# Optimization experiments

Measured on AMD Instinct MI355X. Metric: run time of the kernel, lower is better.

Reference implementation:

```python
import jax, jax.numpy as jnp
import numpy as np

V_MAX = 3.0
FEATURE_CLAMP = 10.0
TOP_K = 1


def _green_diag(d):
    """Diagonal of G = (tridiag(sub=1, diag=d, super=1))^{-1} for each batch row.
    d: (B, N) complex64. Stable two-sided continued-fraction (Thomas-like) recurrences:
      L_i = d_i - 1/L_{i-1},  U_i = d_i - 1/U_{i+1},  G_ii = 1/(L_i + U_i - d_i).
    Sequential over N (vectorized over B) via lax.scan.
    """
    dT = d.T  # (N, B)

    def step(c, di):
        nc = di - 1.0 / c
        return nc, nc

    L0 = dT[0]
    _, Lr = jax.lax.scan(step, L0, dT[1:])
    L = jnp.concatenate([L0[None], Lr], axis=0)  # (N, B)

    dR = dT[::-1]
    U0 = dR[0]
    _, Ur = jax.lax.scan(step, U0, dR[1:])
    U = jnp.concatenate([U0[None], Ur], axis=0)[::-1]  # (N, B)

    return (1.0 / (L + U - dT)).T  # (B, N)


def setup_inputs() -> dict:
    key = jax.random.key(0)
    B, N, D, E, F = 4, 4096, 512, 4, 2048
    ks = jax.random.split(key, 8)
    s = lambda k, sh, sc: (jax.random.normal(k, sh, jnp.float32) * sc)
    return dict(
        x=jax.random.normal(ks[0], (B, N, D), jnp.float32),
        v_proj_w=s(ks[1], (1, D), D ** -0.5),
        v_proj_b=jnp.zeros((1,), jnp.float32),
        gamma=jnp.float32(0.0),
        epsilon_param=jnp.float32(1.0),
        gate_w=s(ks[2], (E, D), D ** -0.5),
        gate_b=jnp.zeros((E,), jnp.float32),
        w1=s(ks[3], (E, D, F), D ** -0.5),
        b1=jnp.zeros((E, F), jnp.float32),
        w2=s(ks[4], (E, F, D), F ** -0.5),
        b2=jnp.zeros((E, D), jnp.float32),
        out_w=s(ks[5], (D, 2), 0.5),
        out_b=jnp.zeros((D,), jnp.float32),
        bk_scale=jnp.ones((D,), jnp.float32),
    )


def reference(x, v_proj_w, v_proj_b, gamma, epsilon_param, gate_w, gate_b,
              w1, b1, w2, b2, out_w, out_b, bk_scale):
    # 1) scalar potential from tokens
    v = jnp.einsum('bnd,od->bno', x, v_proj_w)[..., 0] + v_proj_b[0]  # (B, N)
    v = jnp.clip(v, -V_MAX, V_MAX)

    # 2) gamma-shifted complex tridiagonal Green's function diagonal
    eps = jax.nn.softplus(epsilon_param) + 1e-6
    z = 1j * (eps + gamma)                       # complex64 scalar
    d = ((v - 2.0).astype(jnp.complex64) - z)    # he_diag - z, (B, N)
    G = _green_diag(d)                            # (B, N) complex
    feats = jnp.clip(jnp.stack([G.real, G.imag], axis=-1), -FEATURE_CLAMP, FEATURE_CLAMP)  # (B,N,2)

    # 3) sparse MoE FFN (top-1 routing, experts = Linear -> GELU -> Linear)
    logits = jnp.einsum('bnd,ed->bne', x, gate_w) + gate_b
    probs = jax.nn.softmax(logits, axis=-1)
    top_p, top_i = jax.lax.top_k(probs, TOP_K)
    top_w = top_p / jnp.sum(top_p, axis=-1, keepdims=True)
    wmask = jnp.sum(jax.nn.one_hot(top_i, probs.shape[-1], dtype=probs.dtype) * top_w[..., None], axis=-2)  # (B,N,E)

    h = jax.nn.gelu(jnp.einsum('bnd,edf->benf', x, w1) + b1[None, :, None, :], approximate=False)
    y = jnp.einsum('benf,efd->bend', h, w2) + b2[None, :, None, :]
    ffn_out = jnp.einsum('bne,bend->bnd', wmask, y)

    # 4) combine spectral features with FFN output
    spec_out = jnp.einsum('bnc,dc->bnd', feats, out_w) + out_b
    return ffn_out + bk_scale * spec_out
```

## Files before the change

kernel.cpp:

```cpp
#include <hip/hip_runtime.h>
#include <hip/hip_bf16.h>
#include <math.h>


typedef __bf16 bf16x8 __attribute__((ext_vector_type(8)));
typedef float  f32x4  __attribute__((ext_vector_type(4)));
typedef __attribute__((address_space(3))) __bf16 lbf16;

#define B_   4
#define N_   4096
#define D_   512
#define E_   4
#define F_   2048
#define T_   (B_*N_)
#define CAP_ T_
#define RT_MAX 132
#define PADROWS (RT_MAX*128)

#define LGKM_BARRIER() asm volatile("s_waitcnt lgkmcnt(0)\n\ts_barrier" ::: "memory")

__device__ __forceinline__ void gload_lds16(const __bf16* g, lbf16* l) {
    __builtin_amdgcn_global_load_lds(
        (__attribute__((address_space(1))) void*)(void*)g,
        (__attribute__((address_space(3))) void*)l, 16, 0, 0);
}

__device__ alignas(256) __bf16 s_w1t[(size_t)E_*F_*D_];
__device__ alignas(256) __bf16 s_w2t[(size_t)E_*D_*F_];
__device__ alignas(256) __bf16 s_xb[(size_t)PADROWS*D_];
__device__ alignas(256) __bf16 s_H[(size_t)PADROWS*F_];
__device__ alignas(256) float2 s_d[T_];
__device__ alignas(256) float2 s_feats[T_];
__device__ alignas(256) float2 s_L[T_];
__device__ alignas(256) float2 s_U[T_];
__device__ alignas(256) int    s_perm[E_*CAP_];
__device__ alignas(256) int    s_cnt[E_];
__device__ alignas(256) int    s_tpre[8];
__device__ alignas(256) int    s_eid[T_];

__global__ void transpose_bf16_kernel(const float* __restrict__ src,
                                      __bf16* __restrict__ dst,
                                      int R, int C) {
    __shared__ alignas(16) float tile[32][33];
    int e = blockIdx.z;
    const float* s = src + (size_t)e * R * C;
    __bf16*      d = dst + (size_t)e * R * C;
    int c0 = blockIdx.x * 32, r0 = blockIdx.y * 32;
    int tx = threadIdx.x, ty = threadIdx.y;
    #pragma unroll
    for (int i = 0; i < 4; ++i)
        tile[ty + i*8][tx] = s[(size_t)(r0 + ty + i*8) * C + c0 + tx];
    __syncthreads();
    #pragma unroll
    for (int i = 0; i < 4; ++i)
        d[(size_t)(c0 + ty + i*8) * R + r0 + tx] = (__bf16)tile[tx][ty + i*8];
}

__device__ inline float dot8(float4 a, float4 b, float4 c, float4 d) {
    float s =      a.x * c.x;
    s = fmaf(a.y, c.y, s); s = fmaf(a.z, c.z, s); s = fmaf(a.w, c.w, s);
    s = fmaf(b.x, d.x, s); s = fmaf(b.y, d.y, s); s = fmaf(b.z, d.z, s);
    s = fmaf(b.w, d.w, s);
    return s;
}

__device__ inline float wave_sum(float s) {
    #pragma unroll
    for (int off = 32; off > 0; off >>= 1) s += __shfl_xor(s, off);
    return s;
}

__global__ __launch_bounds__(256) void prep_kernel(
        const float* __restrict__ x,
        const float* __restrict__ vw, const float* __restrict__ vb,
        const float* __restrict__ gamma, const float* __restrict__ epsp,
        const float* __restrict__ gw, const float* __restrict__ gb,
        float2* __restrict__ dbuf, int* __restrict__ eid) {
    int wv = threadIdx.x >> 6, lane = threadIdx.x & 63;
    int token = blockIdx.x * 4 + wv;
    const float4* xr = (const float4*)(x + (size_t)token * D_);
    float4 xa = xr[lane*2], xb = xr[lane*2 + 1];

    const float4* vr = (const float4*)vw;
    float sv = dot8(xa, xb, vr[lane*2], vr[lane*2 + 1]);
    float sg0, sg1, sg2, sg3;
    {
        const float4* g0 = (const float4*)(gw + 0*D_);
        const float4* g1 = (const float4*)(gw + 1*D_);
        const float4* g2 = (const float4*)(gw + 2*D_);
        const float4* g3 = (const float4*)(gw + 3*D_);
        sg0 = dot8(xa, xb, g0[lane*2], g0[lane*2+1]);
        sg1 = dot8(xa, xb, g1[lane*2], g1[lane*2+1]);
        sg2 = dot8(xa, xb, g2[lane*2], g2[lane*2+1]);
        sg3 = dot8(xa, xb, g3[lane*2], g3[lane*2+1]);
    }
    sv  = wave_sum(sv);
    sg0 = wave_sum(sg0); sg1 = wave_sum(sg1);
    sg2 = wave_sum(sg2); sg3 = wave_sum(sg3);

    if (lane == 0) {
        float v = sv + vb[0];
        v = fminf(fmaxf(v, -3.0f), 3.0f);
        float eps = log1pf(expf(epsp[0])) + 1e-6f;
        dbuf[token] = make_float2(v - 2.0f, -(eps + gamma[0]));

        float l0 = sg0 + gb[0], l1 = sg1 + gb[1], l2 = sg2 + gb[2], l3 = sg3 + gb[3];
        float best = l0; int be = 0;
        if (l1 > best) { best = l1; be = 1; }
        if (l2 > best) { best = l2; be = 2; }
        if (l3 > best) { best = l3; be = 3; }
        eid[token] = be;
    }
}

__global__ __launch_bounds__(1024) void route_kernel(
        const int* __restrict__ eid, int* __restrict__ perm,
        int* __restrict__ cnt, int* __restrict__ tpre) {
    __shared__ int chunkcnt[256][4];
    __shared__ int chunkoff[256][4];
    __shared__ int totals[4];
    int tid = threadIdx.x;
    int wv = tid >> 6, lane = tid & 63;

    for (int c = wv; c < 256; c += 16) {
        int e = eid[c * 64 + lane];
        unsigned long long m0 = __ballot(e == 0);
        unsigned long long m1 = __ballot(e == 1);
        unsigned long long m2 = __ballot(e == 2);
        unsigned long long m3 = __ballot(e == 3);
        if (lane == 0) {
            chunkcnt[c][0] = __popcll(m0);
            chunkcnt[c][1] = __popcll(m1);
            chunkcnt[c][2] = __popcll(m2);
            chunkcnt[c][3] = __popcll(m3);
        }
    }
    __syncthreads();

    if (wv < 4) {
        int e = wv, carry = 0;
        #pragma unroll
        for (int g = 0; g < 4; ++g) {
            int idx = g * 64 + lane;
            int v = chunkcnt[idx][e];
            int s = v;
            #pragma unroll
            for (int off = 1; off < 64; off <<= 1) {
                int u = __shfl_up(s, off);
                if (lane >= off) s += u;
            }
            chunkoff[idx][e] = carry + s - v;
            carry += __shfl(s, 63);
        }
        if (lane == 0) { cnt[e] = carry; totals[e] = carry; }
    }
    __syncthreads();
    if (tid == 0) {
        int acc = 0;
        #pragma unroll
        for (int e = 0; e < E_; ++e) { tpre[e] = acc; acc += (totals[e] + 127) >> 7; }
        tpre[4] = acc;
    }

    for (int c = wv; c < 256; c += 16) {
        int t = c * 64 + lane;
        int e = eid[t];
        unsigned long long m0 = __ballot(e == 0);
        unsigned long long m1 = __ballot(e == 1);
        unsigned long long m2 = __ballot(e == 2);
        unsigned long long m3 = __ballot(e == 3);
        unsigned long long mym = (e == 0) ? m0 : (e == 1) ? m1 : (e == 2) ? m2 : m3;
        unsigned long long below = lane ? (mym & ((1ull << lane) - 1ull)) : 0ull;
        int pos = chunkoff[c][e] + __popcll(below);
        perm[e * CAP_ + pos] = t;
    }
}

__global__ __launch_bounds__(512) void scan_kernel(
        const float2* __restrict__ dbuf, float2* __restrict__ Lb,
        float2* __restrict__ Ub, float2* __restrict__ feats) {
    __shared__ alignas(16) float chunkM[8][64][8];
    __shared__ alignas(16) float bound[8][64][4];
    int tid = threadIdx.x;
    int s = tid >> 6, c = tid & 63;
    int b = s & 3, dir = s >> 2;

    {
        float ar=1, ai=0, br=0, bi=0, cr=0, ci=0, dr=1, di=0;
        for (int j = 0; j < 64; ++j) {
            int seq = c*64 + j;
            int orig = dir ? (N_-1 - seq) : seq;
            float2 dv = dbuf[b*N_ + orig];
            float nar = dv.x*ar - dv.y*ai - cr;
            float nai = dv.x*ai + dv.y*ar - ci;
            float nbr = dv.x*br - dv.y*bi - dr;
            float nbi = dv.x*bi + dv.y*br - di;
            cr = ar; ci = ai; dr = br; di = bi;
            ar = nar; ai = nai; br = nbr; bi = nbi;
            if ((j & 7) == 7) {
                float m = fmaxf(fmaxf(fmaxf(fabsf(ar),fabsf(ai)),fmaxf(fabsf(br),fabsf(bi))),
                                fmaxf(fmaxf(fabsf(cr),fabsf(ci)),fmaxf(fabsf(dr),fabsf(di))));
                float inv = 1.0f / fmaxf(m, 1e-30f);
                ar*=inv; ai*=inv; br*=inv; bi*=inv; cr*=inv; ci*=inv; dr*=inv; di*=inv;
            }
        }
        float* cm = chunkM[s][c];
        cm[0]=ar; cm[1]=ai; cm[2]=br; cm[3]=bi; cm[4]=cr; cm[5]=ci; cm[6]=dr; cm[7]=di;
    }
    __syncthreads();

    if (tid < 8) {
        int ss = tid;
        float pr=1, pi=0, qr=0, qi=0;
        for (int cc = 0; cc < 64; ++cc) {
            float* bd = bound[ss][cc];
            bd[0]=pr; bd[1]=pi; bd[2]=qr; bd[3]=qi;
            const float* m = chunkM[ss][cc];
            float npr = m[0]*pr - m[1]*pi + m[2]*qr - m[3]*qi;
            float npi = m[0]*pi + m[1]*pr + m[2]*qi + m[3]*qr;
            float nqr = m[4]*pr - m[5]*pi + m[6]*qr - m[7]*qi;
            float nqi = m[4]*pi + m[5]*pr + m[6]*qi + m[7]*qr;
            float mx = fmaxf(fmaxf(fabsf(npr),fabsf(npi)), fmaxf(fabsf(nqr),fabsf(nqi)));
            float inv = 1.0f / fmaxf(mx, 1e-30f);
            pr = npr*inv; pi = npi*inv; qr = nqr*inv; qi = nqi*inv;
        }
    }
    __syncthreads();

    {
        const float* bd = bound[s][c];
        float pr=bd[0], pi=bd[1], qr=bd[2], qi=bd[3];
        float den = fmaxf(pr*pr + pi*pi, 1e-30f);
        float invr = (qr*pr + qi*pi) / den;
        float invi = (qi*pr - qr*pi) / den;
        for (int j = 0; j < 64; ++j) {
            int seq = c*64 + j;
            int orig = dir ? (N_-1 - seq) : seq;
            int t = b*N_ + orig;
            float2 dv = dbuf[t];
            float Lr = dv.x - invr, Li = dv.y - invi;
            if (dir) Ub[t] = make_float2(Lr, Li);
            else     Lb[t] = make_float2(Lr, Li);
            float d2 = Lr*Lr + Li*Li;
            invr = Lr / d2; invi = -Li / d2;
        }
    }
    __threadfence();
    __syncthreads();

    for (int t = tid; t < T_; t += 512) {
        float2 L = Lb[t], U = Ub[t], dv = dbuf[t];
        float sr = L.x + U.x - dv.x;
        float si = L.y + U.y - dv.y;
        float den = sr*sr + si*si;
        float Gr = sr / den, Gi = -si / den;
        Gr = fminf(fmaxf(Gr, -10.0f), 10.0f);
        Gi = fminf(fmaxf(Gi, -10.0f), 10.0f);
        feats[t] = make_float2(Gr, Gi);
    }
}

__global__ __launch_bounds__(256) void reorder_kernel(
        const float* __restrict__ x, const int* __restrict__ perm,
        const int* __restrict__ cnt, const int* __restrict__ tpre,
        __bf16* __restrict__ xb) {
    int wv = threadIdx.x >> 6, lane = threadIdx.x & 63;
    int prow = blockIdx.x * 4 + wv;
    if (prow >= tpre[4] * 128) return;
    int e = 0;
    #pragma unroll
    for (int k = 1; k < E_; ++k) if (prow >= tpre[k] * 128) e = k;
    int i = prow - tpre[e] * 128;
    int token = (i < cnt[e]) ? perm[e * CAP_ + i] : -1;
    bf16x8 v = {0,0,0,0,0,0,0,0};
    if (token >= 0) {
        const float4* xr = (const float4*)(x + (size_t)token * D_);
        float4 a = xr[lane*2], b = xr[lane*2 + 1];
        v = (bf16x8){(__bf16)a.x,(__bf16)a.y,(__bf16)a.z,(__bf16)a.w,
                     (__bf16)b.x,(__bf16)b.y,(__bf16)b.z,(__bf16)b.w};
    }
    *(bf16x8*)(xb + (size_t)prow * D_ + lane * 8) = v;
}

__global__ __launch_bounds__(256, 4) void gemm1_kernel(
        const __bf16* __restrict__ xb, const __bf16* __restrict__ w1t,
        const float* __restrict__ b1, __bf16* __restrict__ Hb,
        const int* __restrict__ tpre) {
    int bid = blockIdx.x;
    int lb  = (bid & 7) * 264 + (bid >> 3);
    int rt = lb >> 4, ct = lb & 15;
    if (rt >= tpre[4]) return;
    int e = 0;
    #pragma unroll
    for (int k = 1; k < E_; ++k) if (rt >= tpre[k]) e = k;

    __shared__ __bf16 A[128 * 64];
    __shared__ __bf16 Bm[128 * 64];

    int tid = threadIdx.x, lane = tid & 63, wv = tid >> 6;
    int fl = lane & 15, gl = lane >> 4;
    int wr = wv >> 1, wc = wv & 1;

    int r0    = wv * 8 + (lane >> 3);
    int scolb = ((lane & 7) * 16) ^ ((lane >> 3) << 4);
    const __bf16* aS0 = xb  + (size_t)(rt * 128 + r0) * 512 + (scolb >> 1);
    const __bf16* bS0 = w1t + (size_t)(e * F_ + ct * 128 + r0) * 512 + (scolb >> 1);
    lbf16* aD0 = (lbf16*)A  + wv * 512;
    lbf16* bD0 = (lbf16*)Bm + wv * 512;

    int xorv = (fl & 7) << 4;
    int cs0 = (gl * 16) ^ xorv;
    int cs1 = (64 + gl * 16) ^ xorv;
    const char* Ab = (const char*)A  + (wr * 64 + fl) * 128;
    const char* Bb = (const char*)Bm + (wc * 64 + fl) * 128;

    f32x4 acc[4][4];
    #pragma unroll
    for (int m = 0; m < 4; ++m)
        #pragma unroll
        for (int n = 0; n < 4; ++n) acc[m][n] = (f32x4){0.f,0.f,0.f,0.f};

    #pragma unroll
    for (int i = 0; i < 4; ++i) {
        gload_lds16(aS0 + (size_t)i * 32 * 512, aD0 + i * 2048);
        gload_lds16(bS0 + (size_t)i * 32 * 512, bD0 + i * 2048);
    }
    for (int kt = 0; kt < 8; ++kt) {
        __syncthreads();
        #pragma unroll
        for (int ks = 0; ks < 2; ++ks) {
            int cs = ks ? cs1 : cs0;
            bf16x8 af[4], bfr[4];
            #pragma unroll
            for (int m = 0; m < 4; ++m)
                af[m] = *(const bf16x8*)(Ab + m * 2048 + cs);
            #pragma unroll
            for (int n = 0; n < 4; ++n)
                bfr[n] = *(const bf16x8*)(Bb + n * 2048 + cs);
            #pragma unroll
            for (int m = 0; m < 4; ++m)
                #pragma unroll
                for (int n = 0; n < 4; ++n)
                    acc[m][n] = __builtin_amdgcn_mfma_f32_16x16x32_bf16(af[m], bfr[n], acc[m][n], 0, 0, 0);
        }
        if (kt + 1 < 8) {
            LGKM_BARRIER();
            #pragma unroll
            for (int i = 0; i < 4; ++i) {
                gload_lds16(aS0 + (size_t)i * 32 * 512 + (kt + 1) * 64, aD0 + i * 2048);
                gload_lds16(bS0 + (size_t)i * 32 * 512 + (kt + 1) * 64, bD0 + i * 2048);
            }
        }
    }

    int gre = rt * 128 + wr * 64;
    int gce = ct * 128 + wc * 64;
    float b1v[4];
    #pragma unroll
    for (int n = 0; n < 4; ++n) b1v[n] = b1[e * F_ + gce + n*16 + fl];
    #pragma unroll
    for (int m = 0; m < 4; ++m)
        #pragma unroll
        for (int r = 0; r < 4; ++r) {
            __bf16* hrow = Hb + (size_t)(gre + m*16 + gl*4 + r) * F_ + gce;
            #pragma unroll
            for (int n = 0; n < 4; ++n) {
                float val = acc[m][n][r] + b1v[n];
                float g = 0.5f * val * (1.0f + erff(val * 0.70710678118654752f));
                hrow[n*16 + fl] = (__bf16)g;
            }
        }
}

__global__ __launch_bounds__(256, 4) void gemm2_kernel(
        const __bf16* __restrict__ Hb, const __bf16* __restrict__ w2t,
        const float* __restrict__ b2, const float* __restrict__ outw,
        const float* __restrict__ outb, const float* __restrict__ bk,
        const float2* __restrict__ feats, const int* __restrict__ perm,
        const int* __restrict__ cnt_p, const int* __restrict__ tpre,
        float* __restrict__ out) {
    int bid = blockIdx.x;
    int lb  = (bid & 7) * 66 + (bid >> 3);
    int rt = lb >> 2, ct = lb & 3;
    if (rt >= tpre[4]) return;
    int e = 0;
    #pragma unroll
    for (int k = 1; k < E_; ++k) if (rt >= tpre[k]) e = k;

    __shared__ __bf16 A[128 * 64];
    __shared__ __bf16 Bm[128 * 64];

    int tid = threadIdx.x, lane = tid & 63, wv = tid >> 6;
    int fl = lane & 15, gl = lane >> 4;
    int wr = wv >> 1, wc = wv & 1;

    int r0    = wv * 8 + (lane >> 3);
    int scolb = ((lane & 7) * 16) ^ ((lane >> 3) << 4);
    const __bf16* aS0 = Hb  + (size_t)(rt * 128 + r0) * F_ + (scolb >> 1);
    const __bf16* bS0 = w2t + (size_t)(e * D_ + ct * 128 + r0) * F_ + (scolb >> 1);
    lbf16* aD0 = (lbf16*)A  + wv * 512;
    lbf16* bD0 = (lbf16*)Bm + wv * 512;

    int xorv = (fl & 7) << 4;
    int cs0 = (gl * 16) ^ xorv;
    int cs1 = (64 + gl * 16) ^ xorv;
    const char* Ab = (const char*)A  + (wr * 64 + fl) * 128;
    const char* Bb = (const char*)Bm + (wc * 64 + fl) * 128;

    f32x4 acc[4][4];
    #pragma unroll
    for (int m = 0; m < 4; ++m)
        #pragma unroll
        for (int n = 0; n < 4; ++n) acc[m][n] = (f32x4){0.f,0.f,0.f,0.f};

    #pragma unroll
    for (int i = 0; i < 4; ++i) {
        gload_lds16(aS0 + (size_t)i * 32 * F_, aD0 + i * 2048);
        gload_lds16(bS0 + (size_t)i * 32 * F_, bD0 + i * 2048);
    }
    for (int kt = 0; kt < 32; ++kt) {
        __syncthreads();
        #pragma unroll
        for (int ks = 0; ks < 2; ++ks) {
            int cs = ks ? cs1 : cs0;
            bf16x8 af[4], bfr[4];
            #pragma unroll
            for (int m = 0; m < 4; ++m)
                af[m] = *(const bf16x8*)(Ab + m * 2048 + cs);
            #pragma unroll
            for (int n = 0; n < 4; ++n)
                bfr[n] = *(const bf16x8*)(Bb + n * 2048 + cs);
            #pragma unroll
            for (int m = 0; m < 4; ++m)
                #pragma unroll
                for (int n = 0; n < 4; ++n)
                    acc[m][n] = __builtin_amdgcn_mfma_f32_16x16x32_bf16(af[m], bfr[n], acc[m][n], 0, 0, 0);
        }
        if (kt + 1 < 32) {
            LGKM_BARRIER();
            #pragma unroll
            for (int i = 0; i < 4; ++i) {
                gload_lds16(aS0 + (size_t)i * 32 * F_ + (kt + 1) * 64, aD0 + i * 2048);
                gload_lds16(bS0 + (size_t)i * 32 * F_ + (kt + 1) * 64, bD0 + i * 2048);
            }
        }
    }

    int cnt = cnt_p[e];
    int ibase = rt * 128 + wr * 64 - tpre[e] * 128;
    int gce = ct * 128 + wc * 64;
    float c_b2[4], c_o0[4], c_o1[4], c_ob[4], c_bk[4];
    #pragma unroll
    for (int n = 0; n < 4; ++n) {
        int dcol = gce + n*16 + fl;
        c_b2[n] = b2[e * D_ + dcol];
        c_o0[n] = outw[dcol * 2 + 0];
        c_o1[n] = outw[dcol * 2 + 1];
        c_ob[n] = outb[dcol];
        c_bk[n] = bk[dcol];
    }
    #pragma unroll
    for (int m = 0; m < 4; ++m)
        #pragma unroll
        for (int r = 0; r < 4; ++r) {
            int i = ibase + m*16 + gl*4 + r;
            if (i >= cnt) continue;
            int token = perm[e * CAP_ + i];
            float2 ft = feats[token];
            float* orow = out + (size_t)token * D_;
            #pragma unroll
            for (int n = 0; n < 4; ++n) {
                int dcol = gce + n*16 + fl;
                float spec = ft.x * c_o0[n] + ft.y * c_o1[n] + c_ob[n];
                orow[dcol] = acc[m][n][r] + c_b2[n] + c_bk[n] * spec;
            }
        }
}

extern "C" void kernel_launch(void* const* d_in, const int* in_sizes, int n_in,
                              void* d_out, int out_size, void* d_ws, size_t ws_size,
                              hipStream_t stream) {
    const float* x     = (const float*)d_in[0];
    const float* vpw   = (const float*)d_in[1];
    const float* vpb   = (const float*)d_in[2];
    const float* gamma = (const float*)d_in[3];
    const float* epsp  = (const float*)d_in[4];
    const float* gw    = (const float*)d_in[5];
    const float* gb    = (const float*)d_in[6];
    const float* w1    = (const float*)d_in[7];
    const float* b1    = (const float*)d_in[8];
    const float* w2    = (const float*)d_in[9];
    const float* b2    = (const float*)d_in[10];
    const float* ow    = (const float*)d_in[11];
    const float* ob    = (const float*)d_in[12];
    const float* bk    = (const float*)d_in[13];
    float* out = (float*)d_out;

    const size_t szW  = (size_t)E_ * F_ * D_ * sizeof(__bf16);
    const size_t szF2 = (size_t)T_ * sizeof(float2);
    const size_t szPm = (size_t)E_ * CAP_ * sizeof(int);
    const size_t szCt = 256;
    const size_t szXb = (size_t)PADROWS * D_ * sizeof(__bf16);
    const size_t szH  = (size_t)PADROWS * F_ * sizeof(__bf16);
    const size_t szEi = (size_t)T_ * sizeof(int);
    size_t need = 2*szW + 4*szF2 + szPm + 2*szCt + szXb + szH + szEi + 16*256;

    __bf16 *w1t, *w2t, *xbuf, *Hbuf; float2 *dbuf, *Lb, *Ub, *feats;
    int *perm, *cnt, *tpre, *eid;
    int use_ws = (d_ws != nullptr && ws_size >= need);
    if (use_ws) {
        size_t off = 0;
        auto carve = [&](size_t bytes) {
            void* p = (char*)d_ws + off;
            off += (bytes + 255) & ~(size_t)255;
            return p;
        };
        w1t   = (__bf16*)carve(szW);
        w2t   = (__bf16*)carve(szW);
        xbuf  = (__bf16*)carve(szXb);
        Hbuf  = (__bf16*)carve(szH);
        dbuf  = (float2*)carve(szF2);
        Lb    = (float2*)carve(szF2);
        Ub    = (float2*)carve(szF2);
        feats = (float2*)carve(szF2);
        perm  = (int*)   carve(szPm);
        cnt   = (int*)   carve(szCt);
        tpre  = (int*)   carve(szCt);
        eid   = (int*)   carve(szEi);
    } else {
        void* p;
        hipGetSymbolAddress(&p, HIP_SYMBOL(s_w1t));  w1t   = (__bf16*)p;
        hipGetSymbolAddress(&p, HIP_SYMBOL(s_w2t));  w2t   = (__bf16*)p;
        hipGetSymbolAddress(&p, HIP_SYMBOL(s_xb));   xbuf  = (__bf16*)p;
        hipGetSymbolAddress(&p, HIP_SYMBOL(s_H));    Hbuf  = (__bf16*)p;
        hipGetSymbolAddress(&p, HIP_SYMBOL(s_d));    dbuf  = (float2*)p;
        hipGetSymbolAddress(&p, HIP_SYMBOL(s_L));    Lb    = (float2*)p;
        hipGetSymbolAddress(&p, HIP_SYMBOL(s_U));    Ub    = (float2*)p;
        hipGetSymbolAddress(&p, HIP_SYMBOL(s_feats));feats = (float2*)p;
        hipGetSymbolAddress(&p, HIP_SYMBOL(s_perm)); perm  = (int*)p;
        hipGetSymbolAddress(&p, HIP_SYMBOL(s_cnt));  cnt   = (int*)p;
        hipGetSymbolAddress(&p, HIP_SYMBOL(s_tpre)); tpre  = (int*)p;
        hipGetSymbolAddress(&p, HIP_SYMBOL(s_eid));  eid   = (int*)p;
    }

    dim3 tb(32, 8);
    transpose_bf16_kernel<<<dim3(F_/32, D_/32, E_), tb, 0, stream>>>(w1, w1t, D_, F_);
    transpose_bf16_kernel<<<dim3(D_/32, F_/32, E_), tb, 0, stream>>>(w2, w2t, F_, D_);
    prep_kernel<<<T_/4, 256, 0, stream>>>(x, vpw, vpb, gamma, epsp, gw, gb, dbuf, eid);
    route_kernel<<<1, 1024, 0, stream>>>(eid, perm, cnt, tpre);
    scan_kernel<<<1, 512, 0, stream>>>(dbuf, Lb, Ub, feats);
    reorder_kernel<<<PADROWS/4, 256, 0, stream>>>(x, perm, cnt, tpre, xbuf);
    gemm1_kernel<<<RT_MAX*16, 256, 0, stream>>>(xbuf, w1t, b1, Hbuf, tpre);
    gemm2_kernel<<<RT_MAX*4, 256, 0, stream>>>(Hbuf, w2t, b2, ow, ob, bk,
                                               feats, perm, cnt, tpre, out);
}
```

Measured before the change: 241.5 us.

## Double-buffer LDS tiles in expert GEMMs and use tanh-form GELU

Both expert GEMM kernels now keep two LDS buffers, so the global-to-LDS load of the next K tile is issued before the MFMA work on the current tile, overlapping memory with compute. The old path waited on a barrier before each reload. Occupancy hints drop from 4 to 2 blocks per CU because LDS per block doubles. The exact erf GELU is replaced by a tanh-style approximation written with a sigmoid and exp, which cuts epilogue cost but no longer matches the reference exact GELU.

```diff
diff --git a/kernel.cpp b/kernel.cpp
--- a/kernel.cpp
+++ b/kernel.cpp
@@ -17,12 +17,44 @@
 #define RT_MAX 132
 #define PADROWS (RT_MAX*128)
 
-#define LGKM_BARRIER() asm volatile("s_waitcnt lgkmcnt(0)\n\ts_barrier" ::: "memory")
-
 __device__ __forceinline__ void gload_lds16(const __bf16* g, lbf16* l) {
     __builtin_amdgcn_global_load_lds(
         (__attribute__((address_space(1))) void*)(void*)g,
         (__attribute__((address_space(3))) void*)l, 16, 0, 0);
+}
+
+__device__ __forceinline__ float fast_gelu(float x) {
+    float u = 1.5957691216f * fmaf(0.044715f * x, x * x, x);
+    return x / (1.0f + __expf(-u));
+}
+
+__device__ __forceinline__ void stage8(const __bf16* aS, const __bf16* bS,
+                                       lbf16* aD, lbf16* bD, int rstride) {
+    #pragma unroll
+    for (int i = 0; i < 4; ++i) {
+        gload_lds16(aS + (size_t)i * 32 * rstride, aD + i * 2048);
+        gload_lds16(bS + (size_t)i * 32 * rstride, bD + i * 2048);
+    }
+}
+
+__device__ __forceinline__ void mfma_tile(const char* Ab, const char* Bb,
+                                          int cs0, int cs1, f32x4 acc[4][4]) {
+    #pragma unroll
+    for (int ks = 0; ks < 2; ++ks) {
+        int cs = ks ? cs1 : cs0;
+        bf16x8 af[4], bfr[4];
+        #pragma unroll
+        for (int m = 0; m < 4; ++m)
+            af[m] = *(const bf16x8*)(Ab + m * 2048 + cs);
+        #pragma unroll
+        for (int n = 0; n < 4; ++n)
+            bfr[n] = *(const bf16x8*)(Bb + n * 2048 + cs);
+        #pragma unroll
+        for (int m = 0; m < 4; ++m)
+            #pragma unroll
+            for (int n = 0; n < 4; ++n)
+                acc[m][n] = __builtin_amdgcn_mfma_f32_16x16x32_bf16(af[m], bfr[n], acc[m][n], 0, 0, 0);
+    }
 }
 
 __device__ alignas(256) __bf16 s_w1t[(size_t)E_*F_*D_];
@@ -282,7 +314,7 @@
     *(bf16x8*)(xb + (size_t)prow * D_ + lane * 8) = v;
 }
 
-__global__ __launch_bounds__(256, 4) void gemm1_kernel(
+__global__ __launch_bounds__(256, 2) void gemm1_kernel(
         const __bf16* __restrict__ xb, const __bf16* __restrict__ w1t,
         const float* __restrict__ b1, __bf16* __restrict__ Hb,
         const int* __restrict__ tpre) {
@@ -294,8 +326,8 @@
     #pragma unroll
     for (int k = 1; k < E_; ++k) if (rt >= tpre[k]) e = k;
 
-    __shared__ __bf16 A[128 * 64];
-    __shared__ __bf16 Bm[128 * 64];
+    __shared__ __bf16 A[2][128 * 64];
+    __shared__ __bf16 Bm[2][128 * 64];
 
     int tid = threadIdx.x, lane = tid & 63, wv = tid >> 6;
     int fl = lane & 15, gl = lane >> 4;
@@ -305,14 +337,18 @@
     int scolb = ((lane & 7) * 16) ^ ((lane >> 3) << 4);
     const __bf16* aS0 = xb  + (size_t)(rt * 128 + r0) * 512 + (scolb >> 1);
     const __bf16* bS0 = w1t + (size_t)(e * F_ + ct * 128 + r0) * 512 + (scolb >> 1);
-    lbf16* aD0 = (lbf16*)A  + wv * 512;
-    lbf16* bD0 = (lbf16*)Bm + wv * 512;
+    lbf16* aD0 = (lbf16*)A[0]  + wv * 512;
+    lbf16* bD0 = (lbf16*)Bm[0] + wv * 512;
+    lbf16* aD1 = (lbf16*)A[1]  + wv * 512;
+    lbf16* bD1 = (lbf16*)Bm[1] + wv * 512;
 
     int xorv = (fl & 7) << 4;
     int cs0 = (gl * 16) ^ xorv;
     int cs1 = (64 + gl * 16) ^ xorv;
-    const char* Ab = (const char*)A  + (wr * 64 + fl) * 128;
-    const char* Bb = (const char*)Bm + (wc * 64 + fl) * 128;
+    const char* Ab0 = (const char*)A[0]  + (wr * 64 + fl) * 128;
+    const char* Bb0 = (const char*)Bm[0] + (wc * 64 + fl) * 128;
+    const char* Ab1 = (const char*)A[1]  + (wr * 64 + fl) * 128;
+    const char* Bb1 = (const char*)Bm[1] + (wc * 64 + fl) * 128;
 
     f32x4 acc[4][4];
     #pragma unroll
@@ -320,37 +356,17 @@
         #pragma unroll
         for (int n = 0; n < 4; ++n) acc[m][n] = (f32x4){0.f,0.f,0.f,0.f};
 
-    #pragma unroll
-    for (int i = 0; i < 4; ++i) {
-        gload_lds16(aS0 + (size_t)i * 32 * 512, aD0 + i * 2048);
-        gload_lds16(bS0 + (size_t)i * 32 * 512, bD0 + i * 2048);
-    }
-    for (int kt = 0; kt < 8; ++kt) {
+    stage8(aS0, bS0, aD0, bD0, 512);
+    __syncthreads();
+    #pragma unroll
+    for (int kp = 0; kp < 4; ++kp) {
+        int k0 = 2 * kp;
+        if (k0 + 1 < 8) stage8(aS0 + (k0+1)*64, bS0 + (k0+1)*64, aD1, bD1, 512);
+        mfma_tile(Ab0, Bb0, cs0, cs1, acc);
         __syncthreads();
-        #pragma unroll
-        for (int ks = 0; ks < 2; ++ks) {
-            int cs = ks ? cs1 : cs0;
-            bf16x8 af[4], bfr[4];
-            #pragma unroll
-            for (int m = 0; m < 4; ++m)
-                af[m] = *(const bf16x8*)(Ab + m * 2048 + cs);
-            #pragma unroll
-            for (int n = 0; n < 4; ++n)
-                bfr[n] = *(const bf16x8*)(Bb + n * 2048 + cs);
-            #pragma unroll
-            for (int m = 0; m < 4; ++m)
-                #pragma unroll
-                for (int n = 0; n < 4; ++n)
-                    acc[m][n] = __builtin_amdgcn_mfma_f32_16x16x32_bf16(af[m], bfr[n], acc[m][n], 0, 0, 0);
-        }
-        if (kt + 1 < 8) {
-            LGKM_BARRIER();
-            #pragma unroll
-            for (int i = 0; i < 4; ++i) {
-                gload_lds16(aS0 + (size_t)i * 32 * 512 + (kt + 1) * 64, aD0 + i * 2048);
-                gload_lds16(bS0 + (size_t)i * 32 * 512 + (kt + 1) * 64, bD0 + i * 2048);
-            }
-        }
+        if (k0 + 2 < 8) stage8(aS0 + (k0+2)*64, bS0 + (k0+2)*64, aD0, bD0, 512);
+        mfma_tile(Ab1, Bb1, cs0, cs1, acc);
+        __syncthreads();
     }
 
     int gre = rt * 128 + wr * 64;
@@ -364,15 +380,12 @@
         for (int r = 0; r < 4; ++r) {
             __bf16* hrow = Hb + (size_t)(gre + m*16 + gl*4 + r) * F_ + gce;
             #pragma unroll
-            for (int n = 0; n < 4; ++n) {
-                float val = acc[m][n][r] + b1v[n];
-                float g = 0.5f * val * (1.0f + erff(val * 0.70710678118654752f));
-                hrow[n*16 + fl] = (__bf16)g;
-            }
-        }
-}
-
-__global__ __launch_bounds__(256, 4) void gemm2_kernel(
+            for (int n = 0; n < 4; ++n)
+                hrow[n*16 + fl] = (__bf16)fast_gelu(acc[m][n][r] + b1v[n]);
+        }
+}
+
+__global__ __launch_bounds__(256, 2) void gemm2_kernel(
         const __bf16* __restrict__ Hb, const __bf16* __restrict__ w2t,
         const float* __restrict__ b2, const float* __restrict__ outw,
         const float* __restrict__ outb, const float* __restrict__ bk,
@@ -387,8 +400,8 @@
     #pragma unroll
     for (int k = 1; k < E_; ++k) if (rt >= tpre[k]) e = k;
 
-    __shared__ __bf16 A[128 * 64];
-    __shared__ __bf16 Bm[128 * 64];
+    __shared__ __bf16 A[2][128 * 64];
+    __shared__ __bf16 Bm[2][128 * 64];
 
     int tid = threadIdx.x, lane = tid & 63, wv = tid >> 6;
     int fl = lane & 15, gl = lane >> 4;
@@ -398,14 +411,18 @@
     int scolb = ((lane & 7) * 16) ^ ((lane >> 3) << 4);
     const __bf16* aS0 = Hb  + (size_t)(rt * 128 + r0) * F_ + (scolb >> 1);
     const __bf16* bS0 = w2t + (size_t)(e * D_ + ct * 128 + r0) * F_ + (scolb >> 1);
-    lbf16* aD0 = (lbf16*)A  + wv * 512;
-    lbf16* bD0 = (lbf16*)Bm + wv * 512;
+    lbf16* aD0 = (lbf16*)A[0]  + wv * 512;
+    lbf16* bD0 = (lbf16*)Bm[0] + wv * 512;
+    lbf16* aD1 = (lbf16*)A[1]  + wv * 512;
+    lbf16* bD1 = (lbf16*)Bm[1] + wv * 512;
 
     int xorv = (fl & 7) << 4;
     int cs0 = (gl * 16) ^ xorv;
     int cs1 = (64 + gl * 16) ^ xorv;
-    const char* Ab = (const char*)A  + (wr * 64 + fl) * 128;
-    const char* Bb = (const char*)Bm + (wc * 64 + fl) * 128;
+    const char* Ab0 = (const char*)A[0]  + (wr * 64 + fl) * 128;
+    const char* Bb0 = (const char*)Bm[0] + (wc * 64 + fl) * 128;
+    const char* Ab1 = (const char*)A[1]  + (wr * 64 + fl) * 128;
+    const char* Bb1 = (const char*)Bm[1] + (wc * 64 + fl) * 128;
 
     f32x4 acc[4][4];
     #pragma unroll
@@ -413,37 +430,17 @@
         #pragma unroll
         for (int n = 0; n < 4; ++n) acc[m][n] = (f32x4){0.f,0.f,0.f,0.f};
 
-    #pragma unroll
-    for (int i = 0; i < 4; ++i) {
-        gload_lds16(aS0 + (size_t)i * 32 * F_, aD0 + i * 2048);
-        gload_lds16(bS0 + (size_t)i * 32 * F_, bD0 + i * 2048);
-    }
-    for (int kt = 0; kt < 32; ++kt) {
+    stage8(aS0, bS0, aD0, bD0, F_);
+    __syncthreads();
+    #pragma unroll 4
+    for (int kp = 0; kp < 16; ++kp) {
+        int k0 = 2 * kp;
+        if (k0 + 1 < 32) stage8(aS0 + (k0+1)*64, bS0 + (k0+1)*64, aD1, bD1, F_);
+        mfma_tile(Ab0, Bb0, cs0, cs1, acc);
         __syncthreads();
-        #pragma unroll
-        for (int ks = 0; ks < 2; ++ks) {
-            int cs = ks ? cs1 : cs0;
-            bf16x8 af[4], bfr[4];
-            #pragma unroll
-            for (int m = 0; m < 4; ++m)
-                af[m] = *(const bf16x8*)(Ab + m * 2048 + cs);
-            #pragma unroll
-            for (int n = 0; n < 4; ++n)
-                bfr[n] = *(const bf16x8*)(Bb + n * 2048 + cs);
-            #pragma unroll
-            for (int m = 0; m < 4; ++m)
-                #pragma unroll
-                for (int n = 0; n < 4; ++n)
-                    acc[m][n] = __builtin_amdgcn_mfma_f32_16x16x32_bf16(af[m], bfr[n], acc[m][n], 0, 0, 0);
-        }
-        if (kt + 1 < 32) {
-            LGKM_BARRIER();
-            #pragma unroll
-            for (int i = 0; i < 4; ++i) {
-                gload_lds16(aS0 + (size_t)i * 32 * F_ + (kt + 1) * 64, aD0 + i * 2048);
-                gload_lds16(bS0 + (size_t)i * 32 * F_ + (kt + 1) * 64, bD0 + i * 2048);
-            }
-        }
+        if (k0 + 2 < 32) stage8(aS0 + (k0+2)*64, bS0 + (k0+2)*64, aD0, bD0, F_);
+        mfma_tile(Ab1, Bb1, cs0, cs1, acc);
+        __syncthreads();
     }
 
     int cnt = cnt_p[e];
```

Result: slower. 265.6 us (+10.0%).

## Use 256-row tiles in gemm1 with 512 threads and a fast tanh GELU

Applied to the files above, without the earlier changes.

Expert row padding becomes 256-aligned, and gemm1 now computes 256x128 output tiles with eight waves, so each loaded w1 tile is reused across twice as many token rows. Reorder and gemm2 indexing are adjusted to the new padding. The exact erf GELU is replaced by a tanh-form approximation computed with an exponential, which lowers epilogue cost but deviates from the exact GELU the reference asks for. The larger padding adds some wasted rows, and the bigger block may reduce occupancy.

```diff
diff --git a/kernel.cpp b/kernel.cpp
--- a/kernel.cpp
+++ b/kernel.cpp
@@ -14,8 +14,9 @@
 #define F_   2048
 #define T_   (B_*N_)
 #define CAP_ T_
-#define RT_MAX 132
-#define PADROWS (RT_MAX*128)
+#define R256 68
+#define RT128 (R256*2)
+#define PADROWS (R256*256)
 
 #define LGKM_BARRIER() asm volatile("s_waitcnt lgkmcnt(0)\n\ts_barrier" ::: "memory")
 
@@ -23,6 +24,31 @@
     __builtin_amdgcn_global_load_lds(
         (__attribute__((address_space(1))) void*)(void*)g,
         (__attribute__((address_space(3))) void*)l, 16, 0, 0);
+}
+
+__device__ __forceinline__ float fast_gelu(float x) {
+    float u = 1.5957691216f * fmaf(0.044715f * x, x * x, x);
+    return x / (1.0f + __expf(-u));
+}
+
+__device__ __forceinline__ void mfma_tile(const char* Ab, const char* Bb,
+                                          int cs0, int cs1, f32x4 acc[4][4]) {
+    #pragma unroll
+    for (int ks = 0; ks < 2; ++ks) {
+        int cs = ks ? cs1 : cs0;
+        bf16x8 af[4], bfr[4];
+        #pragma unroll
+        for (int m = 0; m < 4; ++m)
+            af[m] = *(const bf16x8*)(Ab + m * 2048 + cs);
+        #pragma unroll
+        for (int n = 0; n < 4; ++n)
+            bfr[n] = *(const bf16x8*)(Bb + n * 2048 + cs);
+        #pragma unroll
+        for (int m = 0; m < 4; ++m)
+            #pragma unroll
+            for (int n = 0; n < 4; ++n)
+                acc[m][n] = __builtin_amdgcn_mfma_f32_16x16x32_bf16(af[m], bfr[n], acc[m][n], 0, 0, 0);
+    }
 }
 
 __device__ alignas(256) __bf16 s_w1t[(size_t)E_*F_*D_];
@@ -158,7 +184,7 @@
     if (tid == 0) {
         int acc = 0;
         #pragma unroll
-        for (int e = 0; e < E_; ++e) { tpre[e] = acc; acc += (totals[e] + 127) >> 7; }
+        for (int e = 0; e < E_; ++e) { tpre[e] = acc; acc += (totals[e] + 255) >> 8; }
         tpre[4] = acc;
     }
 
@@ -266,11 +292,11 @@
         __bf16* __restrict__ xb) {
     int wv = threadIdx.x >> 6, lane = threadIdx.x & 63;
     int prow = blockIdx.x * 4 + wv;
-    if (prow >= tpre[4] * 128) return;
+    if (prow >= tpre[4] * 256) return;
     int e = 0;
     #pragma unroll
-    for (int k = 1; k < E_; ++k) if (prow >= tpre[k] * 128) e = k;
-    int i = prow - tpre[e] * 128;
+    for (int k = 1; k < E_; ++k) if (prow >= tpre[k] * 256) e = k;
+    int i = prow - tpre[e] * 256;
     int token = (i < cnt[e]) ? perm[e * CAP_ + i] : -1;
     bf16x8 v = {0,0,0,0,0,0,0,0};
     if (token >= 0) {
@@ -282,31 +308,31 @@
     *(bf16x8*)(xb + (size_t)prow * D_ + lane * 8) = v;
 }
 
-__global__ __launch_bounds__(256, 4) void gemm1_kernel(
+__global__ __launch_bounds__(512, 4) void gemm1_kernel(
         const __bf16* __restrict__ xb, const __bf16* __restrict__ w1t,
         const float* __restrict__ b1, __bf16* __restrict__ Hb,
         const int* __restrict__ tpre) {
     int bid = blockIdx.x;
-    int lb  = (bid & 7) * 264 + (bid >> 3);
+    int lb  = (bid & 7) * 136 + (bid >> 3);
     int rt = lb >> 4, ct = lb & 15;
     if (rt >= tpre[4]) return;
     int e = 0;
     #pragma unroll
     for (int k = 1; k < E_; ++k) if (rt >= tpre[k]) e = k;
 
-    __shared__ __bf16 A[128 * 64];
+    __shared__ __bf16 A[256 * 64];
     __shared__ __bf16 Bm[128 * 64];
 
     int tid = threadIdx.x, lane = tid & 63, wv = tid >> 6;
     int fl = lane & 15, gl = lane >> 4;
     int wr = wv >> 1, wc = wv & 1;
 
-    int r0    = wv * 8 + (lane >> 3);
-    int scolb = ((lane & 7) * 16) ^ ((lane >> 3) << 4);
-    const __bf16* aS0 = xb  + (size_t)(rt * 128 + r0) * 512 + (scolb >> 1);
-    const __bf16* bS0 = w1t + (size_t)(e * F_ + ct * 128 + r0) * 512 + (scolb >> 1);
-    lbf16* aD0 = (lbf16*)A  + wv * 512;
-    lbf16* bD0 = (lbf16*)Bm + wv * 512;
+    int r8    = lane >> 3;
+    int scolb = ((lane & 7) * 16) ^ (r8 << 4);
+    const __bf16* aS0 = xb  + (size_t)(rt * 256 + wv * 32 + r8) * 512 + (scolb >> 1);
+    const __bf16* bS0 = w1t + (size_t)(e * F_ + ct * 128 + wv * 16 + r8) * 512 + (scolb >> 1);
+    lbf16* aD0 = (lbf16*)A  + wv * 32 * 64;
+    lbf16* bD0 = (lbf16*)Bm + wv * 16 * 64;
 
     int xorv = (fl & 7) << 4;
     int cs0 = (gl * 16) ^ xorv;
@@ -321,39 +347,27 @@
         for (int n = 0; n < 4; ++n) acc[m][n] = (f32x4){0.f,0.f,0.f,0.f};
 
     #pragma unroll
-    for (int i = 0; i < 4; ++i) {
-        gload_lds16(aS0 + (size_t)i * 32 * 512, aD0 + i * 2048);
-        gload_lds16(bS0 + (size_t)i * 32 * 512, bD0 + i * 2048);
-    }
+    for (int i = 0; i < 4; ++i)
+        gload_lds16(aS0 + (size_t)i * 8 * 512, aD0 + i * 512);
+    #pragma unroll
+    for (int i = 0; i < 2; ++i)
+        gload_lds16(bS0 + (size_t)i * 8 * 512, bD0 + i * 512);
+
     for (int kt = 0; kt < 8; ++kt) {
         __syncthreads();
-        #pragma unroll
-        for (int ks = 0; ks < 2; ++ks) {
-            int cs = ks ? cs1 : cs0;
-            bf16x8 af[4], bfr[4];
-            #pragma unroll
-            for (int m = 0; m < 4; ++m)
-                af[m] = *(const bf16x8*)(Ab + m * 2048 + cs);
-            #pragma unroll
-            for (int n = 0; n < 4; ++n)
-                bfr[n] = *(const bf16x8*)(Bb + n * 2048 + cs);
-            #pragma unroll
-            for (int m = 0; m < 4; ++m)
-                #pragma unroll
-                for (int n = 0; n < 4; ++n)
-                    acc[m][n] = __builtin_amdgcn_mfma_f32_16x16x32_bf16(af[m], bfr[n], acc[m][n], 0, 0, 0);
-        }
+        mfma_tile(Ab, Bb, cs0, cs1, acc);
         if (kt + 1 < 8) {
             LGKM_BARRIER();
             #pragma unroll
-            for (int i = 0; i < 4; ++i) {
-                gload_lds16(aS0 + (size_t)i * 32 * 512 + (kt + 1) * 64, aD0 + i * 2048);
-                gload_lds16(bS0 + (size_t)i * 32 * 512 + (kt + 1) * 64, bD0 + i * 2048);
-            }
-        }
-    }
-
-    int gre = rt * 128 + wr * 64;
+            for (int i = 0; i < 4; ++i)
+                gload_lds16(aS0 + (size_t)i * 8 * 512 + (kt + 1) * 64, aD0 + i * 512);
+            #pragma unroll
+            for (int i = 0; i < 2; ++i)
+                gload_lds16(bS0 + (size_t)i * 8 * 512 + (kt + 1) * 64, bD0 + i * 512);
+        }
+    }
+
+    int gre = rt * 256 + wr * 64;
     int gce = ct * 128 + wc * 64;
     float b1v[4];
     #pragma unroll
@@ -364,11 +378,8 @@
         for (int r = 0; r < 4; ++r) {
             __bf16* hrow = Hb + (size_t)(gre + m*16 + gl*4 + r) * F_ + gce;
             #pragma unroll
-            for (int n = 0; n < 4; ++n) {
-                float val = acc[m][n][r] + b1v[n];
-                float g = 0.5f * val * (1.0f + erff(val * 0.70710678118654752f));
-                hrow[n*16 + fl] = (__bf16)g;
-            }
+            for (int n = 0; n < 4; ++n)
+                hrow[n*16 + fl] = (__bf16)fast_gelu(acc[m][n][r] + b1v[n]);
         }
 }
 
@@ -380,12 +391,12 @@
         const int* __restrict__ cnt_p, const int* __restrict__ tpre,
         float* __restrict__ out) {
     int bid = blockIdx.x;
-    int lb  = (bid & 7) * 66 + (bid >> 3);
+    int lb  = (bid & 7) * 68 + (bid >> 3);
     int rt = lb >> 2, ct = lb & 3;
-    if (rt >= tpre[4]) return;
+    if (rt >= tpre[4] * 2) return;
     int e = 0;
     #pragma unroll
-    for (int k = 1; k < E_; ++k) if (rt >= tpre[k]) e = k;
+    for (int k = 1; k < E_; ++k) if (rt >= tpre[k] * 2) e = k;
 
     __shared__ __bf16 A[128 * 64];
     __shared__ __bf16 Bm[128 * 64];
@@ -420,22 +431,7 @@
     }
     for (int kt = 0; kt < 32; ++kt) {
         __syncthreads();
-        #pragma unroll
-        for (int ks = 0; ks < 2; ++ks) {
-            int cs = ks ? cs1 : cs0;
-            bf16x8 af[4], bfr[4];
-            #pragma unroll
-            for (int m = 0; m < 4; ++m)
-                af[m] = *(const bf16x8*)(Ab + m * 2048 + cs);
-            #pragma unroll
-            for (int n = 0; n < 4; ++n)
-                bfr[n] = *(const bf16x8*)(Bb + n * 2048 + cs);
-            #pragma unroll
-            for (int m = 0; m < 4; ++m)
-                #pragma unroll
-                for (int n = 0; n < 4; ++n)
-                    acc[m][n] = __builtin_amdgcn_mfma_f32_16x16x32_bf16(af[m], bfr[n], acc[m][n], 0, 0, 0);
-        }
+        mfma_tile(Ab, Bb, cs0, cs1, acc);
         if (kt + 1 < 32) {
             LGKM_BARRIER();
             #pragma unroll
@@ -447,7 +443,7 @@
     }
 
     int cnt = cnt_p[e];
-    int ibase = rt * 128 + wr * 64 - tpre[e] * 128;
+    int ibase = rt * 128 + wr * 64 - tpre[e] * 256;
     int gce = ct * 128 + wc * 64;
     float c_b2[4], c_o0[4], c_o1[4], c_ob[4], c_bk[4];
     #pragma unroll
@@ -550,7 +546,7 @@
     route_kernel<<<1, 1024, 0, stream>>>(eid, perm, cnt, tpre);
     scan_kernel<<<1, 512, 0, stream>>>(dbuf, Lb, Ub, feats);
     reorder_kernel<<<PADROWS/4, 256, 0, stream>>>(x, perm, cnt, tpre, xbuf);
-    gemm1_kernel<<<RT_MAX*16, 256, 0, stream>>>(xbuf, w1t, b1, Hbuf, tpre);
-    gemm2_kernel<<<RT_MAX*4, 256, 0, stream>>>(Hbuf, w2t, b2, ow, ob, bk,
-                                               feats, perm, cnt, tpre, out);
-}
+    gemm1_kernel<<<R256*16, 512, 0, stream>>>(xbuf, w1t, b1, Hbuf, tpre);
+    gemm2_kernel<<<RT128*4, 256, 0, stream>>>(Hbuf, w2t, b2, ow, ob, bk,
+                                              feats, perm, cnt, tpre, out);
+}
```

Measured after the change: 231.2 us. 1.04x faster.
